# Kernel tuning notes

Measured on AMD Instinct MI355X. Metric: run time of the kernel, lower is better.

The kernel has to match this reference:

```python
import jax, jax.numpy as jnp
import numpy as np

B, N, E, H = 8, 512, 1024, 128   # graphs, nodes, edges, hidden
T = 8                             # num_edge_types
HOPS = 3                          # graph_hops


def setup_inputs() -> dict:
    key = jax.random.key(0)
    ks = jax.random.split(key, 10)
    node_feature = jax.random.normal(ks[0], (B, N, H), dtype=jnp.float32)
    edge_vec = jax.random.randint(ks[1], (B, E), 0, T)  # per-edge type ids
    # sparse incidence matrices (one-hot edge endpoints), as the scipy .A densification does
    src = jax.random.randint(ks[2], (B, E), 0, N)
    tgt = jax.random.randint(ks[3], (B, E), 0, N)
    node2edge = jax.nn.one_hot(src, N, dtype=jnp.float32)                 # [B,E,N]
    edge2node = jnp.swapaxes(jax.nn.one_hot(tgt, N, dtype=jnp.float32), 1, 2)  # [B,N,E]
    s = 0.02  # xavier-ish init scale
    edge_weight_tensor = jax.random.normal(ks[4], (T, H * H), dtype=jnp.float32) * s
    Wz = jax.random.normal(ks[5], (2 * H, H), dtype=jnp.float32) * s
    Wr = jax.random.normal(ks[6], (2 * H, H), dtype=jnp.float32) * s
    Wt = jax.random.normal(ks[7], (2 * H, H), dtype=jnp.float32) * s
    Wf = jax.random.normal(ks[8], (4 * H, H), dtype=jnp.float32) * s
    bf = jnp.zeros((H,), dtype=jnp.float32)
    return {"node_feature": node_feature, "edge_vec": edge_vec,
            "node2edge": node2edge, "edge2node": edge2node,
            "edge_weight_tensor": edge_weight_tensor,
            "Wz": Wz, "Wr": Wr, "Wt": Wt, "Wf": Wf, "bf": bf}


def reference(node_feature, edge_vec, node2edge, edge2node,
              edge_weight_tensor, Wz, Wr, Wt, Wf, bf):
    Hd = node_feature.shape[-1]
    # gather per-edge weight matrices once (edge_vec is constant across hops)
    Wedge = edge_weight_tensor[edge_vec].reshape(edge_vec.shape + (Hd, Hd))  # [B,E,H,H]

    def mp(h, n2e, e2n):
        emb = jnp.einsum('ben,bnh->beh', n2e, h)          # gather node states to edges
        new = jnp.einsum('behd,bed->beh', Wedge, emb)     # per-edge-type matvec
        return jnp.einsum('bne,beh->bnh', e2n, new)       # scatter-aggregate to nodes

    def gru_step(h, a):
        x = jnp.concatenate([h, a], axis=-1)
        z = jax.nn.sigmoid(x @ Wz)
        r = jax.nn.sigmoid(x @ Wr)
        t = jnp.tanh(jnp.concatenate([r * h, a], axis=-1) @ Wt)
        return (1.0 - z) * h + z * t

    h = node_feature
    for _ in range(HOPS):
        bw = mp(h, node2edge, edge2node)
        fw = mp(h, jnp.swapaxes(edge2node, 1, 2), jnp.swapaxes(node2edge, 1, 2))
        # GatedFusion(fw, bw)
        z = jax.nn.sigmoid(jnp.concatenate([fw, bw, fw * bw, fw - bw], axis=-1) @ Wf + bf)
        agg = (1.0 - z) * fw + z * bw
        h = gru_step(h, agg)
    return h
```

## Files before the change

kernel.cpp:

```cpp
#include <hip/hip_runtime.h>

#define Bb 8
#define Nn 512
#define Ee 1024
#define Hh 128
#define Tt 8

#define FG_ROWS 16
#define FG_PAD 132

__device__ __forceinline__ float sigm(float x){ return 1.0f/(1.0f + __expf(-x)); }
__device__ __forceinline__ float tanh_fast(float x){ return 2.0f/(1.0f + __expf(-2.0f*x)) - 1.0f; }

__device__ __forceinline__ void fma4(float* acc, float4 x, float4 w0, float4 w1, float4 w2, float4 w3){
  acc[0] += x.x*w0.x + x.y*w1.x + x.z*w2.x + x.w*w3.x;
  acc[1] += x.x*w0.y + x.y*w1.y + x.z*w2.y + x.w*w3.y;
  acc[2] += x.x*w0.z + x.y*w1.z + x.z*w2.z + x.w*w3.z;
  acc[3] += x.x*w0.w + x.y*w1.w + x.z*w2.w + x.w*w3.w;
}

__global__ void k_extract(const float4* __restrict__ n2e, const float4* __restrict__ e2n,
                          int* __restrict__ src, int* __restrict__ tgt){
  const int total1 = Bb*Ee*Nn/4;
  for (int i = blockIdx.x*blockDim.x + threadIdx.x; i < total1; i += gridDim.x*blockDim.x){
    float4 v = n2e[i];
    if (v.x!=0.f || v.y!=0.f || v.z!=0.f || v.w!=0.f){
      int base = i*4;
      int row = base >> 9;
      int n   = base & 511;
      if (v.x!=0.f) src[row] = n;
      if (v.y!=0.f) src[row] = n+1;
      if (v.z!=0.f) src[row] = n+2;
      if (v.w!=0.f) src[row] = n+3;
    }
  }
  const int total2 = Bb*Nn*Ee/4;
  for (int i = blockIdx.x*blockDim.x + threadIdx.x; i < total2; i += gridDim.x*blockDim.x){
    float4 v = e2n[i];
    if (v.x!=0.f || v.y!=0.f || v.z!=0.f || v.w!=0.f){
      int base = i*4;
      int row = base >> 10;
      int e   = base & 1023;
      int b = row >> 9, n = row & 511;
      int* tp = tgt + b*Ee;
      if (v.x!=0.f) tp[e]   = n;
      if (v.y!=0.f) tp[e+1] = n;
      if (v.z!=0.f) tp[e+2] = n;
      if (v.w!=0.f) tp[e+3] = n;
    }
  }
}

__global__ void k_transW(const float* __restrict__ W, float* __restrict__ WT){
  int i = blockIdx.x*blockDim.x + threadIdx.x;
  if (i >= Tt*Hh*Hh) return;
  int t = i >> 14;
  int h = (i >> 7) & 127;
  int d = i & 127;
  WT[(t*Hh + d)*Hh + h] = W[i];
}

__global__ void k_sort(const int* __restrict__ ev, int* __restrict__ order, int* __restrict__ offs){
  __shared__ int cnt[Tt], offs_s[Tt+1], pos[Tt];
  int b = blockIdx.x, tid = threadIdx.x;
  if (tid < Tt) cnt[tid] = 0;
  __syncthreads();
  for (int e = tid; e < Ee; e += blockDim.x) atomicAdd(&cnt[ev[b*Ee+e]], 1);
  __syncthreads();
  if (tid == 0){ offs_s[0]=0; for (int t=0;t<Tt;t++) offs_s[t+1]=offs_s[t]+cnt[t]; }
  __syncthreads();
  if (tid < Tt) pos[tid] = offs_s[tid];
  if (tid < Tt+1) offs[b*(Tt+1)+tid] = offs_s[tid];
  __syncthreads();
  for (int e = tid; e < Ee; e += blockDim.x){
    int t = ev[b*Ee+e];
    int p = atomicAdd(&pos[t], 1);
    order[b*Ee + p] = e;
  }
}

__global__ __launch_bounds__(256) void k_edge_mp(
    const float* __restrict__ h, const float* __restrict__ WT,
    const int* __restrict__ order, const int* __restrict__ offs,
    const int* __restrict__ src, const int* __restrict__ tgt,
    float* __restrict__ bw, float* __restrict__ fw)
{
  int x = blockIdx.x;
  int dir = x & 1;
  int bt  = x >> 1;
  int t = bt & 7, b = bt >> 3;
  int beg = offs[b*(Tt+1)+t], end = offs[b*(Tt+1)+t+1];
  int chunk0 = beg + blockIdx.y*32;
  if (chunk0 >= end) return;
  const int* gI = dir ? tgt : src;
  const int* sI = dir ? src : tgt;
  float* out = dir ? fw : bw;

  __shared__ float sEmb[32][Hh];
  __shared__ float sW[64][Hh];
  int tid = threadIdx.x;
  int te = tid >> 5, tc = tid & 31;
  int e0 = te*4, c0 = tc*4;
  const float* WTt = WT + t*Hh*Hh;

  for (int chunk = chunk0; chunk < end; chunk += gridDim.y*32){
    int ne = min(32, end - chunk);
    __syncthreads();
    for (int i = tid; i < 32*Hh; i += 256){
      int e = i >> 7, c = i & 127;
      float v = 0.f;
      if (e < ne){
        int eid = order[b*Ee + chunk + e];
        v = h[(b*Nn + gI[b*Ee + eid])*Hh + c];
      }
      sEmb[e][c] = v;
    }
    float acc[4][4] = {};
    for (int kc = 0; kc < Hh; kc += 64){
      __syncthreads();
      for (int i = tid; i < 64*Hh; i += 256){
        int d = i >> 7, c = i & 127;
        sW[d][c] = WTt[(kc + d)*Hh + c];
      }
      __syncthreads();
      #pragma unroll 4
      for (int k = 0; k < 64; k += 4){
        float4 evv[4], wv[4];
        #pragma unroll
        for (int j=0;j<4;j++) evv[j] = *(const float4*)&sEmb[e0+j][kc+k];
        #pragma unroll
        for (int j=0;j<4;j++) wv[j] = *(const float4*)&sW[k+j][c0];
        #pragma unroll
        for (int je=0;je<4;je++) fma4(acc[je], evv[je], wv[0], wv[1], wv[2], wv[3]);
      }
    }
    #pragma unroll
    for (int je=0;je<4;je++){
      int e = e0 + je;
      if (e < ne){
        int eid = order[b*Ee + chunk + e];
        int node = sI[b*Ee + eid];
        float* op = out + (size_t)(b*Nn + node)*Hh + c0;
        atomicAdd(op+0, acc[je][0]);
        atomicAdd(op+1, acc[je][1]);
        atomicAdd(op+2, acc[je][2]);
        atomicAdd(op+3, acc[je][3]);
      }
    }
  }
}


#define CK 32
#define NS 40

__device__ __forceinline__ const float* chunk_ptr(int s, const float* Wf, const float* Wz,
                                                  const float* Wr, const float* Wt){
  if (s < 16) return Wf + s*CK*Hh;
  if (s < 24) return Wz + (s-16)*CK*Hh;
  if (s < 32) return Wr + (s-24)*CK*Hh;
  return Wt + (s-32)*CK*Hh;
}

__device__ __forceinline__ void load_chunk(const float* __restrict__ g, int tid, float4* pf){
  #pragma unroll
  for (int it = 0; it < 2; ++it)
    pf[it] = *(const float4*)(g + (((it<<9) + tid) << 2));
}
__device__ __forceinline__ void write_chunk(float* lds, int tid, const float4* pf){
  #pragma unroll
  for (int it = 0; it < 2; ++it)
    *(float4*)(lds + (((it<<9) + tid) << 2)) = pf[it];
}

__device__ __forceinline__ void chunk_gemm(const float (*X)[FG_PAD], int r, int kb,
                                           const float (*W)[Hh], int col0, float* acc){
  #pragma unroll
  for (int k = 0; k < CK; k += 4){
    float4 x  = *(const float4*)&X[r][kb+k];
    float4 w0 = *(const float4*)&W[k+0][col0];
    float4 w1 = *(const float4*)&W[k+1][col0];
    float4 w2 = *(const float4*)&W[k+2][col0];
    float4 w3 = *(const float4*)&W[k+3][col0];
    fma4(acc, x, w0, w1, w2, w3);
  }
}

__device__ __forceinline__ void chunk_gemm_fuse(const float (*A)[FG_PAD], const float (*B)[FG_PAD],
                                                int mode, int r, int kb, const float (*W)[Hh],
                                                int col0, float* acc){
  #pragma unroll
  for (int k = 0; k < CK; k += 4){
    float4 a = *(const float4*)&A[r][kb+k];
    float4 b = *(const float4*)&B[r][kb+k];
    float4 x;
    if (mode == 0) x = make_float4(a.x*b.x, a.y*b.y, a.z*b.z, a.w*b.w);
    else           x = make_float4(a.x-b.x, a.y-b.y, a.z-b.z, a.w-b.w);
    float4 w0 = *(const float4*)&W[k+0][col0];
    float4 w1 = *(const float4*)&W[k+1][col0];
    float4 w2 = *(const float4*)&W[k+2][col0];
    float4 w3 = *(const float4*)&W[k+3][col0];
    fma4(acc, x, w0, w1, w2, w3);
  }
}

__global__ __launch_bounds__(512) void k_fuse_gru(
    const float* __restrict__ hin, const float* __restrict__ fw, const float* __restrict__ bw,
    const float* __restrict__ Wf, const float* __restrict__ bfv,
    const float* __restrict__ Wz, const float* __restrict__ Wr, const float* __restrict__ Wt,
    float* __restrict__ hout)
{
  __shared__ float sF[FG_ROWS][FG_PAD];
  __shared__ float sS[FG_ROWS][FG_PAD];
  __shared__ float sH[FG_ROWS][FG_PAD];
  __shared__ float sW[2][CK][Hh];

  int tid  = threadIdx.x;
  int row0 = blockIdx.x * FG_ROWS;
  int lane = tid & 63, w = tid >> 6;
  int r    = lane >> 2;
  int col0 = w*16 + (lane & 3)*4;

  float4 pf[2];
  load_chunk(chunk_ptr(0, Wf, Wz, Wr, Wt), tid, pf);

  {
    int ir = tid >> 5;
    int k0 = (tid & 31) << 2;
    size_t gofs = (size_t)(row0 + ir)*Hh + k0;
    float4 fv = *(const float4*)&fw[gofs];
    float4 bv = *(const float4*)&bw[gofs];
    float4 hv = *(const float4*)&hin[gofs];
    *(float4*)&sF[ir][k0] = fv;
    *(float4*)&sS[ir][k0] = bv;
    *(float4*)&sH[ir][k0] = hv;
  }
  float4 bias4 = *(const float4*)&bfv[col0];

  write_chunk(&sW[0][0][0], tid, pf);
  load_chunk(chunk_ptr(1, Wf, Wz, Wr, Wt), tid, pf);
  __syncthreads();

  float af[4] = {0,0,0,0};
  for (int s = 0; s < 16; ++s){
    const float (*Wb)[Hh] = (const float (*)[Hh])sW[s&1];
    int sec = s >> 2, kb = (s & 3)*CK;
    if      (sec == 0) chunk_gemm(sF, r, kb, Wb, col0, af);
    else if (sec == 1) chunk_gemm(sS, r, kb, Wb, col0, af);
    else if (sec == 2) chunk_gemm_fuse(sF, sS, 0, r, kb, Wb, col0, af);
    else               chunk_gemm_fuse(sF, sS, 1, r, kb, Wb, col0, af);
    write_chunk(&sW[(s+1)&1][0][0], tid, pf);
    load_chunk(chunk_ptr(s+2, Wf, Wz, Wr, Wt), tid, pf);
    __syncthreads();
  }

  float agv[4];
  {
    float bb[4] = {bias4.x, bias4.y, bias4.z, bias4.w};
    #pragma unroll
    for (int j = 0; j < 4; ++j){
      float z = sigm(af[j] + bb[j]);
      agv[j] = (1.0f - z)*sF[r][col0+j] + z*sS[r][col0+j];
    }
  }
  *(float4*)&sF[r][col0] = make_float4(agv[0], agv[1], agv[2], agv[3]);
  __syncthreads();

  float az[4] = {0,0,0,0}, ar[4] = {0,0,0,0};
  for (int s = 16; s < 32; ++s){
    const float (*Wb)[Hh] = (const float (*)[Hh])sW[s&1];
    int q = s - 16;
    int kb = (q & 3)*CK;
    const float (*X)[FG_PAD] = ((q & 4) ? sF : sH);
    if (q < 8) chunk_gemm(X, r, kb, Wb, col0, az);
    else       chunk_gemm(X, r, kb, Wb, col0, ar);
    write_chunk(&sW[(s+1)&1][0][0], tid, pf);
    load_chunk(chunk_ptr(s+2, Wf, Wz, Wr, Wt), tid, pf);
    __syncthreads();
  }

  float zz[4];
  {
    float rh[4];
    #pragma unroll
    for (int j = 0; j < 4; ++j){
      zz[j] = sigm(az[j]);
      rh[j] = sigm(ar[j]) * sH[r][col0+j];
    }
    *(float4*)&sS[r][col0] = make_float4(rh[0], rh[1], rh[2], rh[3]);
  }
  __syncthreads();

  float at[4] = {0,0,0,0};
  for (int s = 32; s < NS; ++s){
    const float (*Wb)[Hh] = (const float (*)[Hh])sW[s&1];
    int q = s - 32;
    int kb = (q & 3)*CK;
    const float (*X)[FG_PAD] = ((q & 4) ? sF : sS);
    chunk_gemm(X, r, kb, Wb, col0, at);
    if (s < NS-1){
      write_chunk(&sW[(s+1)&1][0][0], tid, pf);
      if (s < NS-2) load_chunk(chunk_ptr(s+2, Wf, Wz, Wr, Wt), tid, pf);
      __syncthreads();
    }
  }

  float o[4];
  #pragma unroll
  for (int j = 0; j < 4; ++j){
    float t = tanh_fast(at[j]);
    o[j] = (1.0f - zz[j])*sH[r][col0+j] + zz[j]*t;
  }
  *(float4*)&hout[(size_t)(row0 + r)*Hh + col0] = make_float4(o[0], o[1], o[2], o[3]);
}

extern "C" void kernel_launch(void* const* d_in, const int* in_sizes, int n_in,
                              void* d_out, int out_size, void* d_ws, size_t ws_size,
                              hipStream_t stream){
  const float* node_feature = (const float*)d_in[0];
  const int*   edge_vec     = (const int*)d_in[1];
  const float* n2e          = (const float*)d_in[2];
  const float* e2n          = (const float*)d_in[3];
  const float* Wtensor      = (const float*)d_in[4];
  const float* Wz           = (const float*)d_in[5];
  const float* Wr           = (const float*)d_in[6];
  const float* Wt           = (const float*)d_in[7];
  const float* Wf           = (const float*)d_in[8];
  const float* bf           = (const float*)d_in[9];
  float* out = (float*)d_out;

  char* p = (char*)d_ws;
  int* src   = (int*)p; p += Bb*Ee*4;
  int* tgt   = (int*)p; p += Bb*Ee*4;
  int* order = (int*)p; p += Bb*Ee*4;
  int* offs  = (int*)p; p += 4096;
  float* WT  = (float*)p; p += (size_t)Tt*Hh*Hh*4;
  float* bwp = (float*)p; p += (size_t)Bb*Nn*Hh*4;
  float* fwp = (float*)p; p += (size_t)Bb*Nn*Hh*4;
  float* h1  = (float*)p; p += (size_t)Bb*Nn*Hh*4;

  k_extract<<<1024, 256, 0, stream>>>((const float4*)n2e, (const float4*)e2n, src, tgt);
  k_transW<<<(Tt*Hh*Hh + 255)/256, 256, 0, stream>>>(Wtensor, WT);
  k_sort<<<Bb, 256, 0, stream>>>(edge_vec, order, offs);

  const float* hin = node_feature;
  float* houts[3] = { out, h1, out };
  for (int hop = 0; hop < 3; ++hop){
    hipMemsetAsync(bwp, 0, (size_t)2*Bb*Nn*Hh*4, stream);
    k_edge_mp<<<dim3(Bb*Tt*2, 4), 256, 0, stream>>>(hin, WT, order, offs, src, tgt, bwp, fwp);
    k_fuse_gru<<<(Bb*Nn)/FG_ROWS, 512, 0, stream>>>(hin, fwp, bwp, Wf, bf, Wz, Wr, Wt, houts[hop]);
    hin = houts[hop];
  }
}
```

Measured before the change: 477.8 us.

## Fold GatedFusion weights algebraically, read weights from global/L2, fuse accumulator zeroing

```diff
diff --git a/kernel.cpp b/kernel.cpp
--- a/kernel.cpp
+++ b/kernel.cpp
@@ -5,9 +5,7 @@
 #define Ee 1024
 #define Hh 128
 #define Tt 8
-
-#define FG_ROWS 16
-#define FG_PAD 132
+#define FPAD 132
 
 __device__ __forceinline__ float sigm(float x){ return 1.0f/(1.0f + __expf(-x)); }
 __device__ __forceinline__ float tanh_fast(float x){ return 2.0f/(1.0f + __expf(-2.0f*x)) - 1.0f; }
@@ -60,6 +58,17 @@
   WT[(t*Hh + d)*Hh + h] = W[i];
 }
 
+__global__ void k_prep(const float* __restrict__ Wf, float* __restrict__ Ff){
+  int i = blockIdx.x*blockDim.x + threadIdx.x;
+  if (i >= 384*Hh) return;
+  int r = i >> 7, c = i & 127;
+  float v;
+  if (r < 128)      v = Wf[r*Hh + c] + Wf[(r+384)*Hh + c];
+  else if (r < 256) v = Wf[r*Hh + c] - Wf[(r+256)*Hh + c];
+  else              v = Wf[r*Hh + c];
+  Ff[i] = v;
+}
+
 __global__ void k_sort(const int* __restrict__ ev, int* __restrict__ order, int* __restrict__ offs){
   __shared__ int cnt[Tt], offs_s[Tt+1], pos[Tt];
   int b = blockIdx.x, tid = threadIdx.x;
@@ -86,9 +95,7 @@
     float* __restrict__ bw, float* __restrict__ fw)
 {
   int x = blockIdx.x;
-  int dir = x & 1;
-  int bt  = x >> 1;
-  int t = bt & 7, b = bt >> 3;
+  int dir = x & 1, bt = x >> 1, t = bt & 7, b = bt >> 3;
   int beg = offs[b*(Tt+1)+t], end = offs[b*(Tt+1)+t+1];
   int chunk0 = beg + blockIdx.y*32;
   if (chunk0 >= end) return;
@@ -96,188 +103,156 @@
   const int* sI = dir ? src : tgt;
   float* out = dir ? fw : bw;
 
-  __shared__ float sEmb[32][Hh];
-  __shared__ float sW[64][Hh];
-  int tid = threadIdx.x;
-  int te = tid >> 5, tc = tid & 31;
-  int e0 = te*4, c0 = tc*4;
-  const float* WTt = WT + t*Hh*Hh;
+  __shared__ float sEmb[32][FPAD];
+  __shared__ int sNode[32];
+  int tid = threadIdx.x, lane = tid & 63, w = tid >> 6;
+  int e0 = (lane >> 3)*4;
+  int c0 = w*32 + (lane & 7)*4;
+  const float* __restrict__ Wg = WT + t*Hh*Hh + c0;
 
   for (int chunk = chunk0; chunk < end; chunk += gridDim.y*32){
     int ne = min(32, end - chunk);
     __syncthreads();
-    for (int i = tid; i < 32*Hh; i += 256){
-      int e = i >> 7, c = i & 127;
-      float v = 0.f;
-      if (e < ne){
-        int eid = order[b*Ee + chunk + e];
-        v = h[(b*Nn + gI[b*Ee + eid])*Hh + c];
+    {
+      int ir = tid >> 5, k0 = (tid & 31)*4;
+      #pragma unroll
+      for (int rr = 0; rr < 4; ++rr){
+        int e = ir + rr*8;
+        float4 v = {0.f,0.f,0.f,0.f};
+        if (e < ne){
+          int eid = order[b*Ee + chunk + e];
+          v = *(const float4*)&h[(size_t)(b*Nn + gI[b*Ee + eid])*Hh + k0];
+        }
+        *(float4*)&sEmb[e][k0] = v;
       }
-      sEmb[e][c] = v;
-    }
+      if (tid < 32){
+        int nd = -1;
+        if (tid < ne){ int eid = order[b*Ee + chunk + tid]; nd = sI[b*Ee + eid]; }
+        sNode[tid] = nd;
+      }
+    }
+    __syncthreads();
+
     float acc[4][4] = {};
-    for (int kc = 0; kc < Hh; kc += 64){
-      __syncthreads();
-      for (int i = tid; i < 64*Hh; i += 256){
-        int d = i >> 7, c = i & 127;
-        sW[d][c] = WTt[(kc + d)*Hh + c];
+    #pragma unroll 4
+    for (int k = 0; k < Hh; k += 4){
+      float4 w0 = *(const float4*)&Wg[(size_t)(k+0)*Hh];
+      float4 w1 = *(const float4*)&Wg[(size_t)(k+1)*Hh];
+      float4 w2 = *(const float4*)&Wg[(size_t)(k+2)*Hh];
+      float4 w3 = *(const float4*)&Wg[(size_t)(k+3)*Hh];
+      #pragma unroll
+      for (int j = 0; j < 4; ++j){
+        float4 xv = *(const float4*)&sEmb[e0+j][k];
+        fma4(acc[j], xv, w0, w1, w2, w3);
       }
-      __syncthreads();
-      #pragma unroll 4
-      for (int k = 0; k < 64; k += 4){
-        float4 evv[4], wv[4];
-        #pragma unroll
-        for (int j=0;j<4;j++) evv[j] = *(const float4*)&sEmb[e0+j][kc+k];
-        #pragma unroll
-        for (int j=0;j<4;j++) wv[j] = *(const float4*)&sW[k+j][c0];
-        #pragma unroll
-        for (int je=0;je<4;je++) fma4(acc[je], evv[je], wv[0], wv[1], wv[2], wv[3]);
+    }
+    #pragma unroll
+    for (int j = 0; j < 4; ++j){
+      int node = sNode[e0+j];
+      if (node >= 0){
+        float* op = out + (size_t)(b*Nn + node)*Hh + c0;
+        atomicAdd(op+0, acc[j][0]);
+        atomicAdd(op+1, acc[j][1]);
+        atomicAdd(op+2, acc[j][2]);
+        atomicAdd(op+3, acc[j][3]);
       }
     }
-    #pragma unroll
-    for (int je=0;je<4;je++){
-      int e = e0 + je;
-      if (e < ne){
-        int eid = order[b*Ee + chunk + e];
-        int node = sI[b*Ee + eid];
-        float* op = out + (size_t)(b*Nn + node)*Hh + c0;
-        atomicAdd(op+0, acc[je][0]);
-        atomicAdd(op+1, acc[je][1]);
-        atomicAdd(op+2, acc[je][2]);
-        atomicAdd(op+3, acc[je][3]);
-      }
-    }
-  }
-}
-
-
-#define CK 32
-#define NS 40
-
-__device__ __forceinline__ const float* chunk_ptr(int s, const float* Wf, const float* Wz,
-                                                  const float* Wr, const float* Wt){
-  if (s < 16) return Wf + s*CK*Hh;
-  if (s < 24) return Wz + (s-16)*CK*Hh;
-  if (s < 32) return Wr + (s-24)*CK*Hh;
-  return Wt + (s-32)*CK*Hh;
-}
-
-__device__ __forceinline__ void load_chunk(const float* __restrict__ g, int tid, float4* pf){
-  #pragma unroll
-  for (int it = 0; it < 2; ++it)
-    pf[it] = *(const float4*)(g + (((it<<9) + tid) << 2));
-}
-__device__ __forceinline__ void write_chunk(float* lds, int tid, const float4* pf){
-  #pragma unroll
-  for (int it = 0; it < 2; ++it)
-    *(float4*)(lds + (((it<<9) + tid) << 2)) = pf[it];
-}
-
-__device__ __forceinline__ void chunk_gemm(const float (*X)[FG_PAD], int r, int kb,
-                                           const float (*W)[Hh], int col0, float* acc){
-  #pragma unroll
-  for (int k = 0; k < CK; k += 4){
-    float4 x  = *(const float4*)&X[r][kb+k];
-    float4 w0 = *(const float4*)&W[k+0][col0];
-    float4 w1 = *(const float4*)&W[k+1][col0];
-    float4 w2 = *(const float4*)&W[k+2][col0];
-    float4 w3 = *(const float4*)&W[k+3][col0];
+  }
+}
+
+__device__ __forceinline__ void gemm_sec(const float (*X)[FPAD], int r,
+                                         const float* __restrict__ Wg, float* acc){
+  #pragma unroll 4
+  for (int k = 0; k < 128; k += 4){
+    float4 x  = *(const float4*)&X[r][k];
+    float4 w0 = *(const float4*)&Wg[(size_t)(k+0)*Hh];
+    float4 w1 = *(const float4*)&Wg[(size_t)(k+1)*Hh];
+    float4 w2 = *(const float4*)&Wg[(size_t)(k+2)*Hh];
+    float4 w3 = *(const float4*)&Wg[(size_t)(k+3)*Hh];
     fma4(acc, x, w0, w1, w2, w3);
   }
 }
 
-__device__ __forceinline__ void chunk_gemm_fuse(const float (*A)[FG_PAD], const float (*B)[FG_PAD],
-                                                int mode, int r, int kb, const float (*W)[Hh],
-                                                int col0, float* acc){
-  #pragma unroll
-  for (int k = 0; k < CK; k += 4){
-    float4 a = *(const float4*)&A[r][kb+k];
-    float4 b = *(const float4*)&B[r][kb+k];
-    float4 x;
-    if (mode == 0) x = make_float4(a.x*b.x, a.y*b.y, a.z*b.z, a.w*b.w);
-    else           x = make_float4(a.x-b.x, a.y-b.y, a.z-b.z, a.w-b.w);
-    float4 w0 = *(const float4*)&W[k+0][col0];
-    float4 w1 = *(const float4*)&W[k+1][col0];
-    float4 w2 = *(const float4*)&W[k+2][col0];
-    float4 w3 = *(const float4*)&W[k+3][col0];
+__device__ __forceinline__ void gemm_prod(const float (*A)[FPAD], const float (*B)[FPAD], int r,
+                                          const float* __restrict__ Wg, float* acc){
+  #pragma unroll 4
+  for (int k = 0; k < 128; k += 4){
+    float4 a = *(const float4*)&A[r][k];
+    float4 b = *(const float4*)&B[r][k];
+    float4 x = make_float4(a.x*b.x, a.y*b.y, a.z*b.z, a.w*b.w);
+    float4 w0 = *(const float4*)&Wg[(size_t)(k+0)*Hh];
+    float4 w1 = *(const float4*)&Wg[(size_t)(k+1)*Hh];
+    float4 w2 = *(const float4*)&Wg[(size_t)(k+2)*Hh];
+    float4 w3 = *(const float4*)&Wg[(size_t)(k+3)*Hh];
     fma4(acc, x, w0, w1, w2, w3);
+  }
+}
+
+__device__ __forceinline__ void gemm2(const float (*X)[FPAD], int r,
+                                      const float* __restrict__ Wa, const float* __restrict__ Wb,
+                                      float* acc1, float* acc2){
+  #pragma unroll 4
+  for (int k = 0; k < 128; k += 4){
+    float4 x  = *(const float4*)&X[r][k];
+    float4 a0 = *(const float4*)&Wa[(size_t)(k+0)*Hh];
+    float4 a1 = *(const float4*)&Wa[(size_t)(k+1)*Hh];
+    float4 a2 = *(const float4*)&Wa[(size_t)(k+2)*Hh];
+    float4 a3 = *(const float4*)&Wa[(size_t)(k+3)*Hh];
+    fma4(acc1, x, a0, a1, a2, a3);
+    float4 b0 = *(const float4*)&Wb[(size_t)(k+0)*Hh];
+    float4 b1 = *(const float4*)&Wb[(size_t)(k+1)*Hh];
+    float4 b2 = *(const float4*)&Wb[(size_t)(k+2)*Hh];
+    float4 b3 = *(const float4*)&Wb[(size_t)(k+3)*Hh];
+    fma4(acc2, x, b0, b1, b2, b3);
   }
 }
 
 __global__ __launch_bounds__(512) void k_fuse_gru(
     const float* __restrict__ hin, const float* __restrict__ fw, const float* __restrict__ bw,
-    const float* __restrict__ Wf, const float* __restrict__ bfv,
+    const float* __restrict__ Ff, const float* __restrict__ bfv,
     const float* __restrict__ Wz, const float* __restrict__ Wr, const float* __restrict__ Wt,
-    float* __restrict__ hout)
+    float* __restrict__ hout, float* __restrict__ zf, float* __restrict__ zb)
 {
-  __shared__ float sF[FG_ROWS][FG_PAD];
-  __shared__ float sS[FG_ROWS][FG_PAD];
-  __shared__ float sH[FG_ROWS][FG_PAD];
-  __shared__ float sW[2][CK][Hh];
-
+  __shared__ float sF[16][FPAD];
+  __shared__ float sS[16][FPAD];
+  __shared__ float sH[16][FPAD];
   int tid  = threadIdx.x;
-  int row0 = blockIdx.x * FG_ROWS;
+  int row0 = blockIdx.x * 16;
   int lane = tid & 63, w = tid >> 6;
   int r    = lane >> 2;
-  int col0 = w*16 + (lane & 3)*4;
-
-  float4 pf[2];
-  load_chunk(chunk_ptr(0, Wf, Wz, Wr, Wt), tid, pf);
+  int c0   = w*16 + (lane & 3)*4;
 
   {
-    int ir = tid >> 5;
-    int k0 = (tid & 31) << 2;
-    size_t gofs = (size_t)(row0 + ir)*Hh + k0;
-    float4 fv = *(const float4*)&fw[gofs];
-    float4 bv = *(const float4*)&bw[gofs];
-    float4 hv = *(const float4*)&hin[gofs];
-    *(float4*)&sF[ir][k0] = fv;
-    *(float4*)&sS[ir][k0] = bv;
-    *(float4*)&sH[ir][k0] = hv;
-  }
-  float4 bias4 = *(const float4*)&bfv[col0];
-
-  write_chunk(&sW[0][0][0], tid, pf);
-  load_chunk(chunk_ptr(1, Wf, Wz, Wr, Wt), tid, pf);
+    int ir = tid >> 5, k0 = (tid & 31)*4;
+    size_t g = (size_t)(row0 + ir)*Hh + k0;
+    *(float4*)&sF[ir][k0] = *(const float4*)&fw[g];
+    *(float4*)&sS[ir][k0] = *(const float4*)&bw[g];
+    *(float4*)&sH[ir][k0] = *(const float4*)&hin[g];
+  }
+  float4 bias = *(const float4*)&bfv[c0];
   __syncthreads();
 
   float af[4] = {0,0,0,0};
-  for (int s = 0; s < 16; ++s){
-    const float (*Wb)[Hh] = (const float (*)[Hh])sW[s&1];
-    int sec = s >> 2, kb = (s & 3)*CK;
-    if      (sec == 0) chunk_gemm(sF, r, kb, Wb, col0, af);
-    else if (sec == 1) chunk_gemm(sS, r, kb, Wb, col0, af);
-    else if (sec == 2) chunk_gemm_fuse(sF, sS, 0, r, kb, Wb, col0, af);
-    else               chunk_gemm_fuse(sF, sS, 1, r, kb, Wb, col0, af);
-    write_chunk(&sW[(s+1)&1][0][0], tid, pf);
-    load_chunk(chunk_ptr(s+2, Wf, Wz, Wr, Wt), tid, pf);
-    __syncthreads();
-  }
+  gemm_sec (sF, r, Ff + c0,            af);
+  gemm_sec (sS, r, Ff + 128*Hh + c0,   af);
+  gemm_prod(sF, sS, r, Ff + 256*Hh + c0, af);
 
   float agv[4];
   {
-    float bb[4] = {bias4.x, bias4.y, bias4.z, bias4.w};
+    float bb[4] = {bias.x, bias.y, bias.z, bias.w};
     #pragma unroll
     for (int j = 0; j < 4; ++j){
       float z = sigm(af[j] + bb[j]);
-      agv[j] = (1.0f - z)*sF[r][col0+j] + z*sS[r][col0+j];
-    }
-  }
-  *(float4*)&sF[r][col0] = make_float4(agv[0], agv[1], agv[2], agv[3]);
+      agv[j] = (1.0f - z)*sF[r][c0+j] + z*sS[r][c0+j];
+    }
+  }
+  __syncthreads();
+  *(float4*)&sF[r][c0] = make_float4(agv[0], agv[1], agv[2], agv[3]);
   __syncthreads();
 
   float az[4] = {0,0,0,0}, ar[4] = {0,0,0,0};
-  for (int s = 16; s < 32; ++s){
-    const float (*Wb)[Hh] = (const float (*)[Hh])sW[s&1];
-    int q = s - 16;
-    int kb = (q & 3)*CK;
-    const float (*X)[FG_PAD] = ((q & 4) ? sF : sH);
-    if (q < 8) chunk_gemm(X, r, kb, Wb, col0, az);
-    else       chunk_gemm(X, r, kb, Wb, col0, ar);
-    write_chunk(&sW[(s+1)&1][0][0], tid, pf);
-    load_chunk(chunk_ptr(s+2, Wf, Wz, Wr, Wt), tid, pf);
-    __syncthreads();
-  }
+  gemm2(sH, r, Wz + c0,          Wr + c0,          az, ar);
+  gemm2(sF, r, Wz + 128*Hh + c0, Wr + 128*Hh + c0, az, ar);
 
   float zz[4];
   {
@@ -285,33 +260,31 @@
     #pragma unroll
     for (int j = 0; j < 4; ++j){
       zz[j] = sigm(az[j]);
-      rh[j] = sigm(ar[j]) * sH[r][col0+j];
-    }
-    *(float4*)&sS[r][col0] = make_float4(rh[0], rh[1], rh[2], rh[3]);
+      rh[j] = sigm(ar[j]) * sH[r][c0+j];
+    }
+    *(float4*)&sS[r][c0] = make_float4(rh[0], rh[1], rh[2], rh[3]);
   }
   __syncthreads();
 
   float at[4] = {0,0,0,0};
-  for (int s = 32; s < NS; ++s){
-    const float (*Wb)[Hh] = (const float (*)[Hh])sW[s&1];
-    int q = s - 32;
-    int kb = (q & 3)*CK;
-    const float (*X)[FG_PAD] = ((q & 4) ? sF : sS);
-    chunk_gemm(X, r, kb, Wb, col0, at);
-    if (s < NS-1){
-      write_chunk(&sW[(s+1)&1][0][0], tid, pf);
-      if (s < NS-2) load_chunk(chunk_ptr(s+2, Wf, Wz, Wr, Wt), tid, pf);
-      __syncthreads();
-    }
-  }
+  gemm_sec(sS, r, Wt + c0,          at);
+  gemm_sec(sF, r, Wt + 128*Hh + c0, at);
 
   float o[4];
   #pragma unroll
   for (int j = 0; j < 4; ++j){
     float t = tanh_fast(at[j]);
-    o[j] = (1.0f - zz[j])*sH[r][col0+j] + zz[j]*t;
-  }
-  *(float4*)&hout[(size_t)(row0 + r)*Hh + col0] = make_float4(o[0], o[1], o[2], o[3]);
+    o[j] = (1.0f - zz[j])*sH[r][c0+j] + zz[j]*t;
+  }
+  *(float4*)&hout[(size_t)(row0 + r)*Hh + c0] = make_float4(o[0], o[1], o[2], o[3]);
+
+  {
+    int ir = tid >> 5, k0 = (tid & 31)*4;
+    size_t g = (size_t)(row0 + ir)*Hh + k0;
+    float4 zv = {0.f,0.f,0.f,0.f};
+    *(float4*)&zf[g] = zv;
+    *(float4*)&zb[g] = zv;
+  }
 }
 
 extern "C" void kernel_launch(void* const* d_in, const int* in_sizes, int n_in,
@@ -335,20 +308,22 @@
   int* order = (int*)p; p += Bb*Ee*4;
   int* offs  = (int*)p; p += 4096;
   float* WT  = (float*)p; p += (size_t)Tt*Hh*Hh*4;
+  float* Ff  = (float*)p; p += (size_t)384*Hh*4;
   float* bwp = (float*)p; p += (size_t)Bb*Nn*Hh*4;
   float* fwp = (float*)p; p += (size_t)Bb*Nn*Hh*4;
   float* h1  = (float*)p; p += (size_t)Bb*Nn*Hh*4;
 
   k_extract<<<1024, 256, 0, stream>>>((const float4*)n2e, (const float4*)e2n, src, tgt);
   k_transW<<<(Tt*Hh*Hh + 255)/256, 256, 0, stream>>>(Wtensor, WT);
+  k_prep<<<(384*Hh + 255)/256, 256, 0, stream>>>(Wf, Ff);
   k_sort<<<Bb, 256, 0, stream>>>(edge_vec, order, offs);
+  hipMemsetAsync(bwp, 0, (size_t)2*Bb*Nn*Hh*4, stream);
 
   const float* hin = node_feature;
   float* houts[3] = { out, h1, out };
   for (int hop = 0; hop < 3; ++hop){
-    hipMemsetAsync(bwp, 0, (size_t)2*Bb*Nn*Hh*4, stream);
     k_edge_mp<<<dim3(Bb*Tt*2, 4), 256, 0, stream>>>(hin, WT, order, offs, src, tgt, bwp, fwp);
-    k_fuse_gru<<<(Bb*Nn)/FG_ROWS, 512, 0, stream>>>(hin, fwp, bwp, Wf, bf, Wz, Wr, Wt, houts[hop]);
+    k_fuse_gru<<<(Bb*Nn)/16, 512, 0, stream>>>(hin, fwp, bwp, Ff, bf, Wz, Wr, Wt, houts[hop], fwp, bwp);
     hin = houts[hop];
   }
 }
```

New measurement: 474.4 us. Within noise of the previous version (-0.7%).
